# Kernel tuning notes

Measured on AMD Instinct MI355X. Metric: run time of the kernel, lower is better.

## Reference

```python
import jax, jax.numpy as jnp
import numpy as np

JACCARD_THRESH = 0.5
NEGPOS_RATIO = 3
V0, V1 = 0.1, 0.2  # SSD encoding variances


def setup_inputs() -> dict:
    key = jax.random.key(0)
    k1, k2, k3, k4, k5, k6, k7 = jax.random.split(key, 7)
    B, P, C, O = 128, 8732, 21, 16
    loc_data = jax.random.normal(k1, (B, P, 4), dtype=jnp.float32)
    conf_data = jax.random.normal(k2, (B, P, C), dtype=jnp.float32)
    # default boxes in center form (cx, cy, w, h), all in [0,1]
    cxcy = jax.random.uniform(k3, (P, 2), minval=0.05, maxval=0.95)
    wh = jax.random.uniform(k4, (P, 2), minval=0.05, maxval=0.6)
    dbox_list = jnp.concatenate([cxcy, wh], axis=1).astype(jnp.float32)
    # ground-truth boxes in corner form with guaranteed positive extent
    tl = jax.random.uniform(k5, (B, O, 2), minval=0.0, maxval=0.6)
    sz = jax.random.uniform(k6, (B, O, 2), minval=0.05, maxval=0.35)
    labels = jax.random.randint(k7, (B, O, 1), 0, C - 1).astype(jnp.float32)
    targets = jnp.concatenate([tl, tl + sz, labels], axis=2)
    return {"loc_data": loc_data, "conf_data": conf_data,
            "dbox_list": dbox_list, "targets": targets}


def _match_one(truths, labels, dbox):
    """SSD match for one image. truths:[O,4] corner, labels:[O], dbox:[P,4] center."""
    pf = jnp.concatenate([dbox[:, :2] - dbox[:, 2:] * 0.5,
                          dbox[:, :2] + dbox[:, 2:] * 0.5], axis=1)  # point form [P,4]
    lt = jnp.maximum(truths[:, None, :2], pf[None, :, :2])
    rb = jnp.minimum(truths[:, None, 2:], pf[None, :, 2:])
    whi = jnp.clip(rb - lt, 0.0)
    inter = whi[..., 0] * whi[..., 1]                                # [O,P]
    area_t = (truths[:, 2] - truths[:, 0]) * (truths[:, 3] - truths[:, 1])
    area_p = dbox[:, 2] * dbox[:, 3]
    ov = inter / (area_t[:, None] + area_p[None, :] - inter)         # jaccard [O,P]
    best_prior_idx = jnp.argmax(ov, axis=1)                          # [O]
    bto = jnp.max(ov, axis=0)                                        # [P]
    bti = jnp.argmax(ov, axis=0)                                     # [P]
    bto = bto.at[best_prior_idx].set(2.0)
    O = truths.shape[0]
    bti = jax.lax.fori_loop(0, O, lambda j, b: b.at[best_prior_idx[j]].set(j), bti)
    matched = truths[bti]                                            # [P,4]
    conf = labels[bti].astype(jnp.int32) + 1
    conf = jnp.where(bto < JACCARD_THRESH, 0, conf)
    g_cxcy = ((matched[:, :2] + matched[:, 2:]) * 0.5 - dbox[:, :2]) / (V0 * dbox[:, 2:])
    g_wh = jnp.log((matched[:, 2:] - matched[:, :2]) / dbox[:, 2:]) / V1
    return jnp.concatenate([g_cxcy, g_wh], axis=1), conf


def reference(loc_data, conf_data, dbox_list, targets):
    B, P, C = conf_data.shape
    loc_t, conf_t = jax.vmap(_match_one, in_axes=(0, 0, None))(
        targets[..., :4], targets[..., 4], dbox_list)
    pos = conf_t > 0                                                  # [B,P]
    # smooth L1 (beta=1), summed over positives
    ad = jnp.abs(loc_data - loc_t)
    sl1 = jnp.where(ad < 1.0, 0.5 * ad * ad, ad - 0.5)
    loss_l = jnp.sum(jnp.where(pos[..., None], sl1, 0.0))
    # per-prior cross entropy
    logp = jax.nn.log_softmax(conf_data, axis=-1)
    ce = -jnp.take_along_axis(logp, conf_t[..., None], axis=-1)[..., 0]  # [B,P]
    # hard negative mining via double argsort (rank in descending order)
    ce_neg = jnp.where(pos, 0.0, ce)
    loss_idx = jnp.argsort(-ce_neg, axis=1)
    idx_rank = jnp.argsort(loss_idx, axis=1)
    num_pos = jnp.sum(pos, axis=1, keepdims=True)
    num_neg = jnp.minimum(num_pos * NEGPOS_RATIO, P)
    neg = idx_rank < num_neg
    sel = pos | neg
    loss_c = jnp.sum(jnp.where(sel, ce, 0.0))
    N = jnp.sum(num_pos).astype(loc_data.dtype)
    return jnp.stack([loss_l / N, loss_c / N])
```

## Files before the change

kernel.cpp:

```cpp
#include <hip/hip_runtime.h>
#include <cstddef>

#define Bn 128
#define Pn 8732
#define Cn 21
#define On 16
#define MAGIC 0x13579BDFu

__device__ __forceinline__ void argmax_combine(float& v, int& p, float v2, int p2) {
  if (v2 > v || (v2 == v && p2 < p)) { v = v2; p = p2; }
}

__global__ __launch_bounds__(256) void stream_kernel(
    const float* __restrict__ conf, const float* __restrict__ dbox,
    const float* __restrict__ targets,
    float* __restrict__ ce0, unsigned char* __restrict__ pack,
    unsigned long long* __restrict__ keys) {
  const int wb = threadIdx.x >> 6, lane = threadIdx.x & 63;
  const int wave_g = blockIdx.x * 4 + wb;
  const int b = wave_g & 127;
  const int cg = wave_g >> 7;

  __shared__ float4 s_row4[4][336];
  __shared__ float s_tt[4][On * 5];
  __shared__ float s_ar[4][On];

  #pragma unroll
  for (int i = lane; i < On * 5; i += 64)
    s_tt[wb][i] = targets[(size_t)b * On * 5 + i];
  if (lane < On) {
    float x1 = targets[(size_t)b * On * 5 + lane * 5 + 0];
    float y1 = targets[(size_t)b * On * 5 + lane * 5 + 1];
    float x2 = targets[(size_t)b * On * 5 + lane * 5 + 2];
    float y2 = targets[(size_t)b * On * 5 + lane * 5 + 3];
    s_ar[wb][lane] = (x2 - x1) * (y2 - y1);
  }

  float bestv[On]; int bestp[On];
  #pragma unroll
  for (int j = 0; j < On; j++) { bestv[j] = -1.0f; bestp[j] = 0x7fffffff; }

  #pragma unroll
  for (int i = 0; i < 3; i++) {
    const int ci = cg + 64 * i;
    if (ci >= 137) break;
    const int p0 = ci * 64;
    const int rows = min(64, Pn - p0);
    const int n4 = rows * Cn / 4;

    const float4* src = (const float4*)(conf + ((size_t)b * Pn + p0) * Cn);
    float4 v0, v1, v2, v3, v4, v5;
    if (lane < n4)        v0 = src[lane];
    if (lane + 64 < n4)   v1 = src[lane + 64];
    if (lane + 128 < n4)  v2 = src[lane + 128];
    if (lane + 192 < n4)  v3 = src[lane + 192];
    if (lane + 256 < n4)  v4 = src[lane + 256];
    if (lane + 320 < n4)  v5 = src[lane + 320];
    if (lane < n4)        s_row4[wb][lane] = v0;
    if (lane + 64 < n4)   s_row4[wb][lane + 64] = v1;
    if (lane + 128 < n4)  s_row4[wb][lane + 128] = v2;
    if (lane + 192 < n4)  s_row4[wb][lane + 192] = v3;
    if (lane + 256 < n4)  s_row4[wb][lane + 256] = v4;
    if (lane + 320 < n4)  s_row4[wb][lane + 320] = v5;

    if (lane < rows) {
      const int p = p0 + lane;
      const float* x = (const float*)s_row4[wb] + lane * Cn;
      float m = x[0];
      #pragma unroll
      for (int q = 1; q < Cn; q++) m = fmaxf(m, x[q]);
      float s = 0.0f;
      #pragma unroll
      for (int q = 0; q < Cn; q++) s += __expf(x[q] - m);
      float lse = m + __logf(s);
      ce0[(size_t)b * Pn + p] = lse - x[0];

      float4 d = ((const float4*)dbox)[p];
      float px1 = d.x - d.z * 0.5f, py1 = d.y - d.w * 0.5f;
      float px2 = d.x + d.z * 0.5f, py2 = d.y + d.w * 0.5f;
      float ap = d.z * d.w;
      float mv = -1.0f; int mj = 0;
      #pragma unroll
      for (int j = 0; j < On; j++) {
        float lx = fmaxf(s_tt[wb][j*5+0], px1);
        float ly = fmaxf(s_tt[wb][j*5+1], py1);
        float rx = fminf(s_tt[wb][j*5+2], px2);
        float ry = fminf(s_tt[wb][j*5+3], py2);
        float w = fmaxf(rx - lx, 0.0f), h = fmaxf(ry - ly, 0.0f);
        float inter = w * h;
        float ov = __fdividef(inter, s_ar[wb][j] + ap - inter);
        if (ov > bestv[j]) { bestv[j] = ov; bestp[j] = p; }
        if (ov > mv) { mv = ov; mj = j; }
      }
      pack[(size_t)b * Pn + p] =
          (unsigned char)(mj | ((mv >= 0.5f) ? 16 : 0));
    }
  }

  #pragma unroll
  for (int j = 0; j < On; j++) {
    float v = bestv[j]; int p = bestp[j];
    #pragma unroll
    for (int off = 32; off; off >>= 1) {
      float v2 = __shfl_down(v, off);
      int p2 = __shfl_down(p, off);
      argmax_combine(v, p, v2, p2);
    }
    if (lane == 0) {
      unsigned long long key;
      if (v < 0.0f) key = 0xC000000000000000ull;
      else key = (((unsigned long long)(__float_as_uint(v) | 0xC0000000u)) << 32)
               | (unsigned long long)(0xFFFFFFFFu - (unsigned)p);
      atomicMax(&keys[b * On + j], key);
    }
  }
}

__global__ __launch_bounds__(1024) void reduce_kernel(
    const float* __restrict__ loc, const float* __restrict__ conf,
    const float* __restrict__ dbox, const float* __restrict__ targets,
    const float* __restrict__ ce0, const unsigned char* __restrict__ pack,
    const unsigned long long* __restrict__ keys,
    unsigned int* __restrict__ res, float* __restrict__ out) {
  const int b = blockIdx.x;
  const int tid = threadIdx.x;
  const int wave = tid >> 6, lane = tid & 63;

  __shared__ float s_t[On * 5];
  __shared__ int s_bp[On];
  __shared__ unsigned hist[256 * 16];
  __shared__ unsigned s_col[256];
  __shared__ unsigned s_cand[64];
  __shared__ float s_redf[2][16];
  __shared__ int s_redi[16];
  __shared__ unsigned s_prefix;
  __shared__ int s_kk;
  __shared__ int s_cnt;
  __shared__ int s_cc;
  __shared__ int s_np;

  if (tid < On * 5) s_t[tid] = targets[(size_t)b * On * 5 + tid];
  if (tid < On)
    s_bp[tid] = (int)(0xFFFFFFFFu - (unsigned)(keys[b * On + tid] & 0xFFFFFFFFull));
  __syncthreads();

  float ce_r[9];
  float my_loc = 0.0f, my_cep = 0.0f; int my_np = 0;
  #pragma unroll
  for (int sI = 0; sI < 9; sI++) {
    ce_r[sI] = 0.0f;
    const int p = tid + 1024 * sI;
    if (p < Pn) {
      unsigned char pk = pack[(size_t)b * Pn + p];
      float c0 = ce0[(size_t)b * Pn + p];
      int pos = pk >> 4;
      int bt = pk & 15;
      #pragma unroll
      for (int j = 0; j < On; j++)
        if (s_bp[j] == p) { bt = j; pos = 1; }
      ce_r[sI] = pos ? 0.0f : c0;
      if (pos) {
        my_np++;
        const float* t = &s_t[bt * 5];
        int c = (int)t[4] + 1;
        const float* row = conf + ((size_t)b * Pn + p) * Cn;
        my_cep += c0 + row[0] - row[c];
        float4 d = ((const float4*)dbox)[p];
        float mx1 = t[0], my1 = t[1], mx2 = t[2], my2 = t[3];
        float g0 = ((mx1 + mx2) * 0.5f - d.x) / (0.1f * d.z);
        float g1 = ((my1 + my2) * 0.5f - d.y) / (0.1f * d.w);
        float g2 = logf((mx2 - mx1) / d.z) / 0.2f;
        float g3 = logf((my2 - my1) / d.w) / 0.2f;
        float4 ld = ((const float4*)loc)[(size_t)b * Pn + p];
        float g[4] = {g0, g1, g2, g3};
        float l[4] = {ld.x, ld.y, ld.z, ld.w};
        #pragma unroll
        for (int q = 0; q < 4; q++) {
          float ad = fabsf(l[q] - g[q]);
          my_loc += (ad < 1.0f) ? 0.5f * ad * ad : ad - 0.5f;
        }
      }
    }
  }

  {
    int np = my_np;
    #pragma unroll
    for (int off = 32; off; off >>= 1) np += __shfl_down(np, off);
    if (lane == 0) s_redi[wave] = np;
  }
  __syncthreads();
  if (tid == 0) {
    int np = 0;
    #pragma unroll
    for (int w = 0; w < 16; w++) np += s_redi[w];
    s_np = np;
  }
  __syncthreads();

  const int k = min(s_np * 3, Pn);
  unsigned prefix = 0, maskb = 0;
  int kk = k;
  int cntc = Pn;
  for (int shift = 24; shift >= 0; shift -= 8) {
    if (cntc <= 64) break;
    ((uint4*)hist)[tid] = make_uint4(0u, 0u, 0u, 0u);
    __syncthreads();
    #pragma unroll
    for (int sI = 0; sI < 9; sI++) {
      const int p = tid + 1024 * sI;
      if (p < Pn) {
        unsigned u = __float_as_uint(ce_r[sI]);
        if ((u & maskb) == prefix)
          atomicAdd(&hist[(((u >> shift) & 255u) << 4) + (unsigned)wave], 1u);
      }
    }
    __syncthreads();
    if (tid < 256) {
      unsigned c = 0;
      #pragma unroll
      for (int w = 0; w < 16; w++) c += hist[(tid << 4) + w];
      s_col[tid] = c;
    }
    __syncthreads();
    if (tid < 64) {
      unsigned c0 = s_col[4 * tid + 0], c1 = s_col[4 * tid + 1];
      unsigned c2 = s_col[4 * tid + 2], c3 = s_col[4 * tid + 3];
      unsigned t0 = c0 + c1 + c2 + c3;
      unsigned S = t0;
      #pragma unroll
      for (int off = 1; off < 64; off <<= 1) {
        unsigned o = __shfl_down(S, off);
        if (tid + off < 64) S += o;
      }
      unsigned Snext = S - t0;
      unsigned s3 = Snext + c3;
      unsigned s2 = s3 + c2;
      unsigned s1 = s2 + c1;
      unsigned s0 = s1 + c0;
      unsigned kk_u = (unsigned)kk;
      int chosen = -1; unsigned snx = 0, cc = 0;
      if (s3 >= kk_u && Snext < kk_u)      { chosen = 3; snx = Snext; cc = c3; }
      else if (s2 >= kk_u && s3 < kk_u)    { chosen = 2; snx = s3;    cc = c2; }
      else if (s1 >= kk_u && s2 < kk_u)    { chosen = 1; snx = s2;    cc = c1; }
      else if (s0 >= kk_u && s1 < kk_u)    { chosen = 0; snx = s1;    cc = c0; }
      if (chosen >= 0) {
        s_prefix = prefix | ((unsigned)(4 * tid + chosen) << shift);
        s_kk = (int)(kk_u - snx);
        s_cnt = (int)cc;
      }
    }
    __syncthreads();
    prefix = s_prefix; kk = s_kk; cntc = s_cnt;
    maskb |= 255u << shift;
  }
  if (maskb != 0xFFFFFFFFu) {
    if (tid == 0) s_cc = 0;
    __syncthreads();
    #pragma unroll
    for (int sI = 0; sI < 9; sI++) {
      const int p = tid + 1024 * sI;
      if (p < Pn) {
        unsigned u = __float_as_uint(ce_r[sI]);
        if ((u & maskb) == prefix) {
          int ix = atomicAdd(&s_cc, 1);
          s_cand[ix] = u;
        }
      }
    }
    __syncthreads();
    if (tid < 64) {
      int c = s_cc;
      if (tid < c) {
        unsigned v = s_cand[tid];
        int g = 0, e = 0;
        for (int i = 0; i < c; i++) {
          unsigned w = s_cand[i];
          g += (w > v); e += (w == v);
        }
        if (g < kk && kk <= g + e) s_prefix = v;
      }
    }
    __syncthreads();
    prefix = s_prefix;
  }
  float T = __uint_as_float(prefix);

  float sum_gt = 0.0f; int cnt_gt = 0;
  #pragma unroll
  for (int sI = 0; sI < 9; sI++) {
    const int p = tid + 1024 * sI;
    if (p < Pn) {
      float x = ce_r[sI];
      if (x > T) { sum_gt += x; cnt_gt++; }
    }
  }
  #pragma unroll
  for (int off = 32; off; off >>= 1) {
    sum_gt += __shfl_down(sum_gt, off);
    cnt_gt += __shfl_down(cnt_gt, off);
    my_loc += __shfl_down(my_loc, off);
    my_cep += __shfl_down(my_cep, off);
  }
  if (lane == 0) {
    s_redf[0][wave] = my_loc; s_redf[1][wave] = sum_gt + my_cep; s_redi[wave] = cnt_gt;
  }
  __syncthreads();
  if (tid == 0) {
    float ll = 0.0f, lc = 0.0f; int cg = 0;
    #pragma unroll
    for (int w = 0; w < 16; w++) {
      ll += s_redf[0][w]; lc += s_redf[1][w]; cg += s_redi[w];
    }
    lc += (k > 0) ? (float)(k - cg) * T : 0.0f;
    atomicExch(&res[b * 4 + 0], __float_as_uint(ll));
    atomicExch(&res[b * 4 + 1], __float_as_uint(lc));
    atomicExch(&res[b * 4 + 2], (unsigned)s_np);
    __threadfence();
    atomicExch(&res[b * 4 + 3], MAGIC);
  }

  if (b == 0 && tid < 64) {
    float ll = 0.0f, lc = 0.0f; int np = 0;
    #pragma unroll
    for (int h = 0; h < 2; h++) {
      const int i = tid + 64 * h;
      while (atomicAdd(&res[i * 4 + 3], 0u) != MAGIC) { __builtin_amdgcn_s_sleep(8); }
      ll += __uint_as_float(atomicAdd(&res[i * 4 + 0], 0u));
      lc += __uint_as_float(atomicAdd(&res[i * 4 + 1], 0u));
      np += (int)atomicAdd(&res[i * 4 + 2], 0u);
    }
    #pragma unroll
    for (int off = 32; off; off >>= 1) {
      ll += __shfl_down(ll, off);
      lc += __shfl_down(lc, off);
      np += __shfl_down(np, off);
    }
    if (tid == 0) {
      float fN = (float)np;
      out[0] = ll / fN;
      out[1] = lc / fN;
    }
  }
}

extern "C" void kernel_launch(void* const* d_in, const int* in_sizes, int n_in,
                              void* d_out, int out_size, void* d_ws, size_t ws_size,
                              hipStream_t stream) {
  const float* loc_data  = (const float*)d_in[0];
  const float* conf_data = (const float*)d_in[1];
  const float* dbox      = (const float*)d_in[2];
  const float* targets   = (const float*)d_in[3];
  float* out = (float*)d_out;

  char* ws = (char*)d_ws;
  float* ce0 = (float*)ws;
  unsigned char* pack = (unsigned char*)(ws + (size_t)Bn * Pn * 4);
  unsigned long long* keys =
      (unsigned long long*)(ws + (size_t)Bn * Pn * 5);
  unsigned int* res = (unsigned int*)(ws + (size_t)Bn * Pn * 5 + Bn * On * 8);

  stream_kernel<<<2048, 256, 0, stream>>>(conf_data, dbox, targets, ce0, pack, keys);
  reduce_kernel<<<Bn, 1024, 0, stream>>>(loc_data, conf_data, dbox, targets,
                                         ce0, pack, keys, res, out);
}
```

Baseline: 205.2 us.

## Software-pipeline conf chunk loads in registers ahead of compute in stream kernel

Restructures the per-wave chunk loop so the global loads for the first two conf chunks are issued up front into register buffers, and the third chunk's load is issued before the second chunk is computed. This lets global memory latency overlap with the softmax and IoU compute instead of being serialized per chunk. Target loads are also hoisted into registers before the conf loads and written to shared memory afterward. The cost is higher register pressure from holding two 6-float4 buffers, which may reduce occupancy.

Measured after the change: 252.4 us. +23.0%, slower.

```diff
diff --git a/kernel.cpp b/kernel.cpp
--- a/kernel.cpp
+++ b/kernel.cpp
@@ -25,44 +25,58 @@
   __shared__ float s_tt[4][On * 5];
   __shared__ float s_ar[4][On];
 
-  #pragma unroll
-  for (int i = lane; i < On * 5; i += 64)
-    s_tt[wb][i] = targets[(size_t)b * On * 5 + i];
+  const size_t tb = (size_t)b * On * 5;
+  float tva = targets[tb + lane];
+  float tvb = 0.0f, ax1 = 0.0f, ay1 = 0.0f, ax2 = 0.0f, ay2 = 0.0f;
   if (lane < On) {
-    float x1 = targets[(size_t)b * On * 5 + lane * 5 + 0];
-    float y1 = targets[(size_t)b * On * 5 + lane * 5 + 1];
-    float x2 = targets[(size_t)b * On * 5 + lane * 5 + 2];
-    float y2 = targets[(size_t)b * On * 5 + lane * 5 + 3];
-    s_ar[wb][lane] = (x2 - x1) * (y2 - y1);
-  }
-
-  float bestv[On]; int bestp[On];
-  #pragma unroll
-  for (int j = 0; j < On; j++) { bestv[j] = -1.0f; bestp[j] = 0x7fffffff; }
-
-  #pragma unroll
-  for (int i = 0; i < 3; i++) {
-    const int ci = cg + 64 * i;
-    if (ci >= 137) break;
+    tvb = targets[tb + 64 + lane];
+    ax1 = targets[tb + lane * 5 + 0];
+    ay1 = targets[tb + lane * 5 + 1];
+    ax2 = targets[tb + lane * 5 + 2];
+    ay2 = targets[tb + lane * 5 + 3];
+  }
+
+  float4 ra[6], rb[6];
+  auto LOADR = [&](float4 (&r)[6], int ci) {
     const int p0 = ci * 64;
     const int rows = min(64, Pn - p0);
     const int n4 = rows * Cn / 4;
-
     const float4* src = (const float4*)(conf + ((size_t)b * Pn + p0) * Cn);
-    float4 v0, v1, v2, v3, v4, v5;
-    if (lane < n4)        v0 = src[lane];
-    if (lane + 64 < n4)   v1 = src[lane + 64];
-    if (lane + 128 < n4)  v2 = src[lane + 128];
-    if (lane + 192 < n4)  v3 = src[lane + 192];
-    if (lane + 256 < n4)  v4 = src[lane + 256];
-    if (lane + 320 < n4)  v5 = src[lane + 320];
-    if (lane < n4)        s_row4[wb][lane] = v0;
-    if (lane + 64 < n4)   s_row4[wb][lane + 64] = v1;
-    if (lane + 128 < n4)  s_row4[wb][lane + 128] = v2;
-    if (lane + 192 < n4)  s_row4[wb][lane + 192] = v3;
-    if (lane + 256 < n4)  s_row4[wb][lane + 256] = v4;
-    if (lane + 320 < n4)  s_row4[wb][lane + 320] = v5;
-
+    if (lane < n4)        r[0] = src[lane];
+    if (lane + 64 < n4)   r[1] = src[lane + 64];
+    if (lane + 128 < n4)  r[2] = src[lane + 128];
+    if (lane + 192 < n4)  r[3] = src[lane + 192];
+    if (lane + 256 < n4)  r[4] = src[lane + 256];
+    if (lane + 320 < n4)  r[5] = src[lane + 320];
+  };
+  auto WRITER = [&](const float4 (&r)[6], int ci) {
+    const int p0 = ci * 64;
+    const int rows = min(64, Pn - p0);
+    const int n4 = rows * Cn / 4;
+    if (lane < n4)        s_row4[wb][lane] = r[0];
+    if (lane + 64 < n4)   s_row4[wb][lane + 64] = r[1];
+    if (lane + 128 < n4)  s_row4[wb][lane + 128] = r[2];
+    if (lane + 192 < n4)  s_row4[wb][lane + 192] = r[3];
+    if (lane + 256 < n4)  s_row4[wb][lane + 256] = r[4];
+    if (lane + 320 < n4)  s_row4[wb][lane + 320] = r[5];
+  };
+
+  LOADR(ra, cg);
+  LOADR(rb, cg + 64);
+
+  s_tt[wb][lane] = tva;
+  if (lane < On) {
+    s_tt[wb][64 + lane] = tvb;
+    s_ar[wb][lane] = (ax2 - ax1) * (ay2 - ay1);
+  }
+
+  float bestv[On]; int bestp[On];
+  #pragma unroll
+  for (int j = 0; j < On; j++) { bestv[j] = -1.0f; bestp[j] = 0x7fffffff; }
+
+  auto COMPUTE = [&](int ci) {
+    const int p0 = ci * 64;
+    const int rows = min(64, Pn - p0);
     if (lane < rows) {
       const int p = p0 + lane;
       const float* x = (const float*)s_row4[wb] + lane * Cn;
@@ -95,7 +109,15 @@
       pack[(size_t)b * Pn + p] =
           (unsigned char)(mj | ((mv >= 0.5f) ? 16 : 0));
     }
-  }
+  };
+
+  WRITER(ra, cg);
+  COMPUTE(cg);
+  WRITER(rb, cg + 64);
+  const bool has2 = (cg < 9);
+  if (has2) LOADR(ra, cg + 128);
+  COMPUTE(cg + 64);
+  if (has2) { WRITER(ra, cg + 128); COMPUTE(cg + 128); }
 
   #pragma unroll
   for (int j = 0; j < On; j++) {
```

## Fuse stream and reduce kernels via last-arriving-block per-image reduction

Applied to the files above, without the earlier changes.

Merges the two kernels into one launch. The last wave to finish streaming an image, found with an atomic counter, runs that image's top-k reduction inside a 256-thread block. A second counter picks the final block to do the global sum. The stream grid shrinks from 64 to 32 waves per image, each covering up to 5 chunks, and shared memory is overlaid with a union. The aim is to remove the kernel-launch gap and the spin-wait, but the per-image reduction now runs with 256 threads instead of 1024 and adds a memset. Key buffers are not reset, as before.

New measurement: 436.2 us. +112.6%, slower.

```diff
diff --git a/kernel.cpp b/kernel.cpp
--- a/kernel.cpp
+++ b/kernel.cpp
@@ -5,151 +5,55 @@
 #define Pn 8732
 #define Cn 21
 #define On 16
-#define MAGIC 0x13579BDFu
+#define NW 32
+#define NI 35
 
 __device__ __forceinline__ void argmax_combine(float& v, int& p, float v2, int p2) {
   if (v2 > v || (v2 == v && p2 < p)) { v = v2; p = p2; }
 }
 
-__global__ __launch_bounds__(256) void stream_kernel(
-    const float* __restrict__ conf, const float* __restrict__ dbox,
-    const float* __restrict__ targets,
-    float* __restrict__ ce0, unsigned char* __restrict__ pack,
-    unsigned long long* __restrict__ keys) {
-  const int wb = threadIdx.x >> 6, lane = threadIdx.x & 63;
-  const int wave_g = blockIdx.x * 4 + wb;
-  const int b = wave_g & 127;
-  const int cg = wave_g >> 7;
-
-  __shared__ float4 s_row4[4][336];
-  __shared__ float s_tt[4][On * 5];
-  __shared__ float s_ar[4][On];
-
-  #pragma unroll
-  for (int i = lane; i < On * 5; i += 64)
-    s_tt[wb][i] = targets[(size_t)b * On * 5 + i];
-  if (lane < On) {
-    float x1 = targets[(size_t)b * On * 5 + lane * 5 + 0];
-    float y1 = targets[(size_t)b * On * 5 + lane * 5 + 1];
-    float x2 = targets[(size_t)b * On * 5 + lane * 5 + 2];
-    float y2 = targets[(size_t)b * On * 5 + lane * 5 + 3];
-    s_ar[wb][lane] = (x2 - x1) * (y2 - y1);
-  }
-
-  float bestv[On]; int bestp[On];
-  #pragma unroll
-  for (int j = 0; j < On; j++) { bestv[j] = -1.0f; bestp[j] = 0x7fffffff; }
-
-  #pragma unroll
-  for (int i = 0; i < 3; i++) {
-    const int ci = cg + 64 * i;
-    if (ci >= 137) break;
-    const int p0 = ci * 64;
-    const int rows = min(64, Pn - p0);
-    const int n4 = rows * Cn / 4;
-
-    const float4* src = (const float4*)(conf + ((size_t)b * Pn + p0) * Cn);
-    float4 v0, v1, v2, v3, v4, v5;
-    if (lane < n4)        v0 = src[lane];
-    if (lane + 64 < n4)   v1 = src[lane + 64];
-    if (lane + 128 < n4)  v2 = src[lane + 128];
-    if (lane + 192 < n4)  v3 = src[lane + 192];
-    if (lane + 256 < n4)  v4 = src[lane + 256];
-    if (lane + 320 < n4)  v5 = src[lane + 320];
-    if (lane < n4)        s_row4[wb][lane] = v0;
-    if (lane + 64 < n4)   s_row4[wb][lane + 64] = v1;
-    if (lane + 128 < n4)  s_row4[wb][lane + 128] = v2;
-    if (lane + 192 < n4)  s_row4[wb][lane + 192] = v3;
-    if (lane + 256 < n4)  s_row4[wb][lane + 256] = v4;
-    if (lane + 320 < n4)  s_row4[wb][lane + 320] = v5;
-
-    if (lane < rows) {
-      const int p = p0 + lane;
-      const float* x = (const float*)s_row4[wb] + lane * Cn;
-      float m = x[0];
-      #pragma unroll
-      for (int q = 1; q < Cn; q++) m = fmaxf(m, x[q]);
-      float s = 0.0f;
-      #pragma unroll
-      for (int q = 0; q < Cn; q++) s += __expf(x[q] - m);
-      float lse = m + __logf(s);
-      ce0[(size_t)b * Pn + p] = lse - x[0];
-
-      float4 d = ((const float4*)dbox)[p];
-      float px1 = d.x - d.z * 0.5f, py1 = d.y - d.w * 0.5f;
-      float px2 = d.x + d.z * 0.5f, py2 = d.y + d.w * 0.5f;
-      float ap = d.z * d.w;
-      float mv = -1.0f; int mj = 0;
-      #pragma unroll
-      for (int j = 0; j < On; j++) {
-        float lx = fmaxf(s_tt[wb][j*5+0], px1);
-        float ly = fmaxf(s_tt[wb][j*5+1], py1);
-        float rx = fminf(s_tt[wb][j*5+2], px2);
-        float ry = fminf(s_tt[wb][j*5+3], py2);
-        float w = fmaxf(rx - lx, 0.0f), h = fmaxf(ry - ly, 0.0f);
-        float inter = w * h;
-        float ov = __fdividef(inter, s_ar[wb][j] + ap - inter);
-        if (ov > bestv[j]) { bestv[j] = ov; bestp[j] = p; }
-        if (ov > mv) { mv = ov; mj = j; }
-      }
-      pack[(size_t)b * Pn + p] =
-          (unsigned char)(mj | ((mv >= 0.5f) ? 16 : 0));
-    }
-  }
-
-  #pragma unroll
-  for (int j = 0; j < On; j++) {
-    float v = bestv[j]; int p = bestp[j];
-    #pragma unroll
-    for (int off = 32; off; off >>= 1) {
-      float v2 = __shfl_down(v, off);
-      int p2 = __shfl_down(p, off);
-      argmax_combine(v, p, v2, p2);
-    }
-    if (lane == 0) {
-      unsigned long long key;
-      if (v < 0.0f) key = 0xC000000000000000ull;
-      else key = (((unsigned long long)(__float_as_uint(v) | 0xC0000000u)) << 32)
-               | (unsigned long long)(0xFFFFFFFFu - (unsigned)p);
-      atomicMax(&keys[b * On + j], key);
-    }
-  }
-}
-
-__global__ __launch_bounds__(1024) void reduce_kernel(
+union SmemU {
+  struct {
+    float4 row4[4][336];
+    float  tt[4][On * 5];
+    float  ar[4][On];
+  } st;
+  struct {
+    unsigned hist[256 * 4];
+    unsigned col[256];
+    unsigned cand[64];
+    float    t[On * 5];
+    int      bp[On];
+    float    redf[2][4];
+    int      redi[4];
+    unsigned prefix;
+    int      kk, cnt, cc, np, fin;
+  } rd;
+};
+
+__device__ void reduce_image(
+    int b, SmemU& u,
     const float* __restrict__ loc, const float* __restrict__ conf,
     const float* __restrict__ dbox, const float* __restrict__ targets,
     const float* __restrict__ ce0, const unsigned char* __restrict__ pack,
     const unsigned long long* __restrict__ keys,
-    unsigned int* __restrict__ res, float* __restrict__ out) {
-  const int b = blockIdx.x;
+    unsigned* res, unsigned* done2, float* out) {
   const int tid = threadIdx.x;
   const int wave = tid >> 6, lane = tid & 63;
 
-  __shared__ float s_t[On * 5];
-  __shared__ int s_bp[On];
-  __shared__ unsigned hist[256 * 16];
-  __shared__ unsigned s_col[256];
-  __shared__ unsigned s_cand[64];
-  __shared__ float s_redf[2][16];
-  __shared__ int s_redi[16];
-  __shared__ unsigned s_prefix;
-  __shared__ int s_kk;
-  __shared__ int s_cnt;
-  __shared__ int s_cc;
-  __shared__ int s_np;
-
-  if (tid < On * 5) s_t[tid] = targets[(size_t)b * On * 5 + tid];
+  __threadfence();
+
+  if (tid < On * 5) u.rd.t[tid] = targets[(size_t)b * On * 5 + tid];
   if (tid < On)
-    s_bp[tid] = (int)(0xFFFFFFFFu - (unsigned)(keys[b * On + tid] & 0xFFFFFFFFull));
-  __syncthreads();
-
-  float ce_r[9];
+    u.rd.bp[tid] = (int)(0xFFFFFFFFu - (unsigned)(keys[b * On + tid] & 0xFFFFFFFFull));
+  __syncthreads();
+
+  float ce_r[NI];
   float my_loc = 0.0f, my_cep = 0.0f; int my_np = 0;
   #pragma unroll
-  for (int sI = 0; sI < 9; sI++) {
+  for (int sI = 0; sI < NI; sI++) {
     ce_r[sI] = 0.0f;
-    const int p = tid + 1024 * sI;
+    const int p = tid + 256 * sI;
     if (p < Pn) {
       unsigned char pk = pack[(size_t)b * Pn + p];
       float c0 = ce0[(size_t)b * Pn + p];
@@ -157,11 +61,11 @@
       int bt = pk & 15;
       #pragma unroll
       for (int j = 0; j < On; j++)
-        if (s_bp[j] == p) { bt = j; pos = 1; }
+        if (u.rd.bp[j] == p) { bt = j; pos = 1; }
       ce_r[sI] = pos ? 0.0f : c0;
       if (pos) {
         my_np++;
-        const float* t = &s_t[bt * 5];
+        const float* t = &u.rd.t[bt * 5];
         int c = (int)t[4] + 1;
         const float* row = conf + ((size_t)b * Pn + p) * Cn;
         my_cep += c0 + row[0] - row[c];
@@ -187,45 +91,40 @@
     int np = my_np;
     #pragma unroll
     for (int off = 32; off; off >>= 1) np += __shfl_down(np, off);
-    if (lane == 0) s_redi[wave] = np;
-  }
-  __syncthreads();
-  if (tid == 0) {
-    int np = 0;
-    #pragma unroll
-    for (int w = 0; w < 16; w++) np += s_redi[w];
-    s_np = np;
-  }
-  __syncthreads();
-
-  const int k = min(s_np * 3, Pn);
+    if (lane == 0) u.rd.redi[wave] = np;
+  }
+  __syncthreads();
+  if (tid == 0)
+    u.rd.np = u.rd.redi[0] + u.rd.redi[1] + u.rd.redi[2] + u.rd.redi[3];
+  __syncthreads();
+
+  const int k = min(u.rd.np * 3, Pn);
   unsigned prefix = 0, maskb = 0;
   int kk = k;
   int cntc = Pn;
   for (int shift = 24; shift >= 0; shift -= 8) {
     if (cntc <= 64) break;
-    ((uint4*)hist)[tid] = make_uint4(0u, 0u, 0u, 0u);
-    __syncthreads();
-    #pragma unroll
-    for (int sI = 0; sI < 9; sI++) {
-      const int p = tid + 1024 * sI;
+    ((uint4*)u.rd.hist)[tid] = make_uint4(0u, 0u, 0u, 0u);
+    __syncthreads();
+    #pragma unroll
+    for (int sI = 0; sI < NI; sI++) {
+      const int p = tid + 256 * sI;
       if (p < Pn) {
-        unsigned u = __float_as_uint(ce_r[sI]);
-        if ((u & maskb) == prefix)
-          atomicAdd(&hist[(((u >> shift) & 255u) << 4) + (unsigned)wave], 1u);
-      }
-    }
-    __syncthreads();
-    if (tid < 256) {
-      unsigned c = 0;
-      #pragma unroll
-      for (int w = 0; w < 16; w++) c += hist[(tid << 4) + w];
-      s_col[tid] = c;
+        unsigned uu = __float_as_uint(ce_r[sI]);
+        if ((uu & maskb) == prefix)
+          atomicAdd(&u.rd.hist[(((uu >> shift) & 255u) << 2) + (unsigned)wave], 1u);
+      }
+    }
+    __syncthreads();
+    {
+      unsigned c = u.rd.hist[tid * 4 + 0] + u.rd.hist[tid * 4 + 1] +
+                   u.rd.hist[tid * 4 + 2] + u.rd.hist[tid * 4 + 3];
+      u.rd.col[tid] = c;
     }
     __syncthreads();
     if (tid < 64) {
-      unsigned c0 = s_col[4 * tid + 0], c1 = s_col[4 * tid + 1];
-      unsigned c2 = s_col[4 * tid + 2], c3 = s_col[4 * tid + 3];
+      unsigned c0 = u.rd.col[4 * tid + 0], c1 = u.rd.col[4 * tid + 1];
+      unsigned c2 = u.rd.col[4 * tid + 2], c3 = u.rd.col[4 * tid + 3];
       unsigned t0 = c0 + c1 + c2 + c3;
       unsigned S = t0;
       #pragma unroll
@@ -245,51 +144,51 @@
       else if (s1 >= kk_u && s2 < kk_u)    { chosen = 1; snx = s2;    cc = c1; }
       else if (s0 >= kk_u && s1 < kk_u)    { chosen = 0; snx = s1;    cc = c0; }
       if (chosen >= 0) {
-        s_prefix = prefix | ((unsigned)(4 * tid + chosen) << shift);
-        s_kk = (int)(kk_u - snx);
-        s_cnt = (int)cc;
-      }
-    }
-    __syncthreads();
-    prefix = s_prefix; kk = s_kk; cntc = s_cnt;
+        u.rd.prefix = prefix | ((unsigned)(4 * tid + chosen) << shift);
+        u.rd.kk = (int)(kk_u - snx);
+        u.rd.cnt = (int)cc;
+      }
+    }
+    __syncthreads();
+    prefix = u.rd.prefix; kk = u.rd.kk; cntc = u.rd.cnt;
     maskb |= 255u << shift;
   }
   if (maskb != 0xFFFFFFFFu) {
-    if (tid == 0) s_cc = 0;
-    __syncthreads();
-    #pragma unroll
-    for (int sI = 0; sI < 9; sI++) {
-      const int p = tid + 1024 * sI;
+    if (tid == 0) u.rd.cc = 0;
+    __syncthreads();
+    #pragma unroll
+    for (int sI = 0; sI < NI; sI++) {
+      const int p = tid + 256 * sI;
       if (p < Pn) {
-        unsigned u = __float_as_uint(ce_r[sI]);
-        if ((u & maskb) == prefix) {
-          int ix = atomicAdd(&s_cc, 1);
-          s_cand[ix] = u;
+        unsigned uu = __float_as_uint(ce_r[sI]);
+        if ((uu & maskb) == prefix) {
+          int ix = atomicAdd(&u.rd.cc, 1);
+          u.rd.cand[ix] = uu;
         }
       }
     }
     __syncthreads();
     if (tid < 64) {
-      int c = s_cc;
+      int c = u.rd.cc;
       if (tid < c) {
-        unsigned v = s_cand[tid];
+        unsigned v = u.rd.cand[tid];
         int g = 0, e = 0;
         for (int i = 0; i < c; i++) {
-          unsigned w = s_cand[i];
+          unsigned w = u.rd.cand[i];
           g += (w > v); e += (w == v);
         }
-        if (g < kk && kk <= g + e) s_prefix = v;
-      }
-    }
-    __syncthreads();
-    prefix = s_prefix;
+        if (g < kk && kk <= g + e) u.rd.prefix = v;
+      }
+    }
+    __syncthreads();
+    prefix = u.rd.prefix;
   }
   float T = __uint_as_float(prefix);
 
   float sum_gt = 0.0f; int cnt_gt = 0;
   #pragma unroll
-  for (int sI = 0; sI < 9; sI++) {
-    const int p = tid + 1024 * sI;
+  for (int sI = 0; sI < NI; sI++) {
+    const int p = tid + 256 * sI;
     if (p < Pn) {
       float x = ce_r[sI];
       if (x > T) { sum_gt += x; cnt_gt++; }
@@ -303,32 +202,33 @@
     my_cep += __shfl_down(my_cep, off);
   }
   if (lane == 0) {
-    s_redf[0][wave] = my_loc; s_redf[1][wave] = sum_gt + my_cep; s_redi[wave] = cnt_gt;
+    u.rd.redf[0][wave] = my_loc;
+    u.rd.redf[1][wave] = sum_gt + my_cep;
+    u.rd.redi[wave] = cnt_gt;
   }
   __syncthreads();
   if (tid == 0) {
-    float ll = 0.0f, lc = 0.0f; int cg = 0;
-    #pragma unroll
-    for (int w = 0; w < 16; w++) {
-      ll += s_redf[0][w]; lc += s_redf[1][w]; cg += s_redi[w];
-    }
-    lc += (k > 0) ? (float)(k - cg) * T : 0.0f;
+    float ll = 0.0f, lc = 0.0f; int cg2 = 0;
+    #pragma unroll
+    for (int w = 0; w < 4; w++) {
+      ll += u.rd.redf[0][w]; lc += u.rd.redf[1][w]; cg2 += u.rd.redi[w];
+    }
+    lc += (k > 0) ? (float)(k - cg2) * T : 0.0f;
     atomicExch(&res[b * 4 + 0], __float_as_uint(ll));
     atomicExch(&res[b * 4 + 1], __float_as_uint(lc));
-    atomicExch(&res[b * 4 + 2], (unsigned)s_np);
+    atomicExch(&res[b * 4 + 2], (unsigned)u.rd.np);
     __threadfence();
-    atomicExch(&res[b * 4 + 3], MAGIC);
-  }
-
-  if (b == 0 && tid < 64) {
+    unsigned o2 = atomicAdd(done2, 1u);
+    u.rd.fin = (o2 == (unsigned)(Bn - 1)) ? 1 : 0;
+  }
+  __syncthreads();
+  if (u.rd.fin) {
+    __threadfence();
     float ll = 0.0f, lc = 0.0f; int np = 0;
-    #pragma unroll
-    for (int h = 0; h < 2; h++) {
-      const int i = tid + 64 * h;
-      while (atomicAdd(&res[i * 4 + 3], 0u) != MAGIC) { __builtin_amdgcn_s_sleep(8); }
-      ll += __uint_as_float(atomicAdd(&res[i * 4 + 0], 0u));
-      lc += __uint_as_float(atomicAdd(&res[i * 4 + 1], 0u));
-      np += (int)atomicAdd(&res[i * 4 + 2], 0u);
+    if (tid < Bn) {
+      ll = __uint_as_float(atomicAdd(&res[tid * 4 + 0], 0u));
+      lc = __uint_as_float(atomicAdd(&res[tid * 4 + 1], 0u));
+      np = (int)atomicAdd(&res[tid * 4 + 2], 0u);
     }
     #pragma unroll
     for (int off = 32; off; off >>= 1) {
@@ -336,11 +236,140 @@
       lc += __shfl_down(lc, off);
       np += __shfl_down(np, off);
     }
+    if (lane == 0 && wave < 2) {
+      u.rd.redf[0][wave] = ll; u.rd.redf[1][wave] = lc; u.rd.redi[wave] = np;
+    }
+    __syncthreads();
     if (tid == 0) {
-      float fN = (float)np;
-      out[0] = ll / fN;
-      out[1] = lc / fN;
-    }
+      float L = u.rd.redf[0][0] + u.rd.redf[0][1];
+      float C = u.rd.redf[1][0] + u.rd.redf[1][1];
+      float N = (float)(u.rd.redi[0] + u.rd.redi[1]);
+      out[0] = L / N;
+      out[1] = C / N;
+    }
+  }
+  __syncthreads();
+}
+
+__global__ __launch_bounds__(256) void fused_kernel(
+    const float* __restrict__ loc, const float* __restrict__ conf,
+    const float* __restrict__ dbox, const float* __restrict__ targets,
+    float* __restrict__ ce0, unsigned char* __restrict__ pack,
+    unsigned long long* __restrict__ keys,
+    unsigned* __restrict__ res, float* __restrict__ out) {
+  const int wb = threadIdx.x >> 6, lane = threadIdx.x & 63;
+  const int wave_g = blockIdx.x * 4 + wb;
+  const int b = wave_g & 127;
+  const int cg = wave_g >> 7;
+
+  unsigned* done  = res + Bn * 4;
+  unsigned* done2 = done + Bn;
+
+  __shared__ SmemU u;
+  __shared__ int s_job[4];
+
+  #pragma unroll
+  for (int i = lane; i < On * 5; i += 64)
+    u.st.tt[wb][i] = targets[(size_t)b * On * 5 + i];
+  if (lane < On) {
+    float x1 = targets[(size_t)b * On * 5 + lane * 5 + 0];
+    float y1 = targets[(size_t)b * On * 5 + lane * 5 + 1];
+    float x2 = targets[(size_t)b * On * 5 + lane * 5 + 2];
+    float y2 = targets[(size_t)b * On * 5 + lane * 5 + 3];
+    u.st.ar[wb][lane] = (x2 - x1) * (y2 - y1);
+  }
+
+  float bestv[On]; int bestp[On];
+  #pragma unroll
+  for (int j = 0; j < On; j++) { bestv[j] = -1.0f; bestp[j] = 0x7fffffff; }
+
+  #pragma unroll
+  for (int i = 0; i < 5; i++) {
+    const int ci = cg + 32 * i;
+    if (ci >= 137) break;
+    const int p0 = ci * 64;
+    const int rows = min(64, Pn - p0);
+    const int n4 = rows * Cn / 4;
+
+    const float4* src = (const float4*)(conf + ((size_t)b * Pn + p0) * Cn);
+    float4 v0, v1, v2, v3, v4, v5;
+    if (lane < n4)        v0 = src[lane];
+    if (lane + 64 < n4)   v1 = src[lane + 64];
+    if (lane + 128 < n4)  v2 = src[lane + 128];
+    if (lane + 192 < n4)  v3 = src[lane + 192];
+    if (lane + 256 < n4)  v4 = src[lane + 256];
+    if (lane + 320 < n4)  v5 = src[lane + 320];
+    if (lane < n4)        u.st.row4[wb][lane] = v0;
+    if (lane + 64 < n4)   u.st.row4[wb][lane + 64] = v1;
+    if (lane + 128 < n4)  u.st.row4[wb][lane + 128] = v2;
+    if (lane + 192 < n4)  u.st.row4[wb][lane + 192] = v3;
+    if (lane + 256 < n4)  u.st.row4[wb][lane + 256] = v4;
+    if (lane + 320 < n4)  u.st.row4[wb][lane + 320] = v5;
+
+    if (lane < rows) {
+      const int p = p0 + lane;
+      const float* x = (const float*)u.st.row4[wb] + lane * Cn;
+      float m = x[0];
+      #pragma unroll
+      for (int q = 1; q < Cn; q++) m = fmaxf(m, x[q]);
+      float s = 0.0f;
+      #pragma unroll
+      for (int q = 0; q < Cn; q++) s += __expf(x[q] - m);
+      float lse = m + __logf(s);
+      ce0[(size_t)b * Pn + p] = lse - x[0];
+
+      float4 d = ((const float4*)dbox)[p];
+      float px1 = d.x - d.z * 0.5f, py1 = d.y - d.w * 0.5f;
+      float px2 = d.x + d.z * 0.5f, py2 = d.y + d.w * 0.5f;
+      float ap = d.z * d.w;
+      float mv = -1.0f; int mj = 0;
+      #pragma unroll
+      for (int j = 0; j < On; j++) {
+        float lx = fmaxf(u.st.tt[wb][j*5+0], px1);
+        float ly = fmaxf(u.st.tt[wb][j*5+1], py1);
+        float rx = fminf(u.st.tt[wb][j*5+2], px2);
+        float ry = fminf(u.st.tt[wb][j*5+3], py2);
+        float w = fmaxf(rx - lx, 0.0f), h = fmaxf(ry - ly, 0.0f);
+        float inter = w * h;
+        float ov = __fdividef(inter, u.st.ar[wb][j] + ap - inter);
+        if (ov > bestv[j]) { bestv[j] = ov; bestp[j] = p; }
+        if (ov > mv) { mv = ov; mj = j; }
+      }
+      pack[(size_t)b * Pn + p] =
+          (unsigned char)(mj | ((mv >= 0.5f) ? 16 : 0));
+    }
+  }
+
+  #pragma unroll
+  for (int j = 0; j < On; j++) {
+    float v = bestv[j]; int p = bestp[j];
+    #pragma unroll
+    for (int off = 32; off; off >>= 1) {
+      float v2 = __shfl_down(v, off);
+      int p2 = __shfl_down(p, off);
+      argmax_combine(v, p, v2, p2);
+    }
+    if (lane == 0) {
+      unsigned long long key;
+      if (v < 0.0f) key = 0xC000000000000000ull;
+      else key = (((unsigned long long)(__float_as_uint(v) | 0xC0000000u)) << 32)
+               | (unsigned long long)(0xFFFFFFFFu - (unsigned)p);
+      atomicMax(&keys[b * On + j], key);
+    }
+  }
+
+  if (lane == 0) {
+    __threadfence();
+    unsigned old = atomicAdd(&done[b], 1u);
+    s_job[wb] = (old == (unsigned)(NW - 1)) ? b : -1;
+  }
+  __syncthreads();
+
+  for (int s = 0; s < 4; ++s) {
+    const int img = s_job[s];
+    if (img >= 0)
+      reduce_image(img, u, loc, conf, dbox, targets, ce0, pack, keys,
+                   res, done2, out);
   }
 }
 
@@ -358,9 +387,11 @@
   unsigned char* pack = (unsigned char*)(ws + (size_t)Bn * Pn * 4);
   unsigned long long* keys =
       (unsigned long long*)(ws + (size_t)Bn * Pn * 5);
-  unsigned int* res = (unsigned int*)(ws + (size_t)Bn * Pn * 5 + Bn * On * 8);
-
-  stream_kernel<<<2048, 256, 0, stream>>>(conf_data, dbox, targets, ce0, pack, keys);
-  reduce_kernel<<<Bn, 1024, 0, stream>>>(loc_data, conf_data, dbox, targets,
-                                         ce0, pack, keys, res, out);
+  unsigned int* res =
+      (unsigned int*)(ws + (size_t)Bn * Pn * 5 + Bn * On * 8);
+
+  hipMemsetAsync(res, 0, (size_t)(Bn * 4 + Bn + 1) * sizeof(unsigned), stream);
+
+  fused_kernel<<<Bn * NW / 4, 256, 0, stream>>>(
+      loc_data, conf_data, dbox, targets, ce0, pack, keys, res, out);
 }
```

## Fuse positive-prior loss accumulation into stream kernel and vectorize reduce pass

Applied to the files above, without the earlier changes.

Positive-prior localization and confidence losses are now computed in the streaming kernel while the conf row is already in shared memory, and accumulated per image with atomics. The reduce kernel only corrects for the forced best-prior matches and loads ce0 as float4 instead of re-scanning pack, conf and loc per prior. Grid size is halved so each wave processes more chunks. This adds a memset, float atomics (non-deterministic summation order) and a correction path for duplicate best-prior indices.

Result: slower. 210.3 us (+2.5%).

```diff
diff --git a/kernel.cpp b/kernel.cpp
--- a/kernel.cpp
+++ b/kernel.cpp
@@ -11,11 +11,25 @@
   if (v2 > v || (v2 == v && p2 < p)) { v = v2; p = p2; }
 }
 
+__device__ __forceinline__ float sl1_enc(float4 lv, float4 d,
+                                         float t0, float t1, float t2, float t3) {
+  float g0 = ((t0 + t2) * 0.5f - d.x) / (0.1f * d.z);
+  float g1 = ((t1 + t3) * 0.5f - d.y) / (0.1f * d.w);
+  float g2 = __logf((t2 - t0) / d.z) / 0.2f;
+  float g3 = __logf((t3 - t1) / d.w) / 0.2f;
+  float r = 0.f, a;
+  a = fabsf(lv.x - g0); r += (a < 1.f) ? 0.5f * a * a : a - 0.5f;
+  a = fabsf(lv.y - g1); r += (a < 1.f) ? 0.5f * a * a : a - 0.5f;
+  a = fabsf(lv.z - g2); r += (a < 1.f) ? 0.5f * a * a : a - 0.5f;
+  a = fabsf(lv.w - g3); r += (a < 1.f) ? 0.5f * a * a : a - 0.5f;
+  return r;
+}
+
 __global__ __launch_bounds__(256) void stream_kernel(
-    const float* __restrict__ conf, const float* __restrict__ dbox,
-    const float* __restrict__ targets,
+    const float* __restrict__ loc, const float* __restrict__ conf,
+    const float* __restrict__ dbox, const float* __restrict__ targets,
     float* __restrict__ ce0, unsigned char* __restrict__ pack,
-    unsigned long long* __restrict__ keys) {
+    unsigned long long* __restrict__ keys, unsigned* __restrict__ part) {
   const int wb = threadIdx.x >> 6, lane = threadIdx.x & 63;
   const int wave_g = blockIdx.x * 4 + wb;
   const int b = wave_g & 127;
@@ -25,7 +39,6 @@
   __shared__ float s_tt[4][On * 5];
   __shared__ float s_ar[4][On];
 
-  #pragma unroll
   for (int i = lane; i < On * 5; i += 64)
     s_tt[wb][i] = targets[(size_t)b * On * 5 + i];
   if (lane < On) {
@@ -40,9 +53,11 @@
   #pragma unroll
   for (int j = 0; j < On; j++) { bestv[j] = -1.0f; bestp[j] = 0x7fffffff; }
 
-  #pragma unroll
-  for (int i = 0; i < 3; i++) {
-    const int ci = cg + 64 * i;
+  float acc_loc = 0.0f, acc_cep = 0.0f; int acc_np = 0;
+
+  #pragma unroll
+  for (int i = 0; i < 5; i++) {
+    const int ci = cg + 32 * i;
     if (ci >= 137) break;
     const int p0 = ci * 64;
     const int rows = min(64, Pn - p0);
@@ -73,7 +88,6 @@
       #pragma unroll
       for (int q = 0; q < Cn; q++) s += __expf(x[q] - m);
       float lse = m + __logf(s);
-      ce0[(size_t)b * Pn + p] = lse - x[0];
 
       float4 d = ((const float4*)dbox)[p];
       float px1 = d.x - d.z * 0.5f, py1 = d.y - d.w * 0.5f;
@@ -92,9 +106,31 @@
         if (ov > bestv[j]) { bestv[j] = ov; bestp[j] = p; }
         if (ov > mv) { mv = ov; mj = j; }
       }
-      pack[(size_t)b * Pn + p] =
-          (unsigned char)(mj | ((mv >= 0.5f) ? 16 : 0));
-    }
+      const bool pos = (mv >= 0.5f);
+      pack[(size_t)b * Pn + p] = (unsigned char)(mj | (pos ? 16 : 0));
+      ce0[(size_t)b * Pn + p] = pos ? 0.0f : (lse - x[0]);
+
+      if (pos) {
+        acc_np++;
+        int c = (int)s_tt[wb][mj * 5 + 4] + 1;
+        acc_cep += lse - x[c];
+        float4 lv = ((const float4*)loc)[(size_t)b * Pn + p];
+        acc_loc += sl1_enc(lv, d, s_tt[wb][mj*5+0], s_tt[wb][mj*5+1],
+                                  s_tt[wb][mj*5+2], s_tt[wb][mj*5+3]);
+      }
+    }
+  }
+
+  #pragma unroll
+  for (int off = 32; off; off >>= 1) {
+    acc_loc += __shfl_down(acc_loc, off);
+    acc_cep += __shfl_down(acc_cep, off);
+    acc_np  += __shfl_down(acc_np, off);
+  }
+  if (lane == 0) {
+    atomicAdd((float*)&part[b * 4 + 0], acc_loc);
+    atomicAdd((float*)&part[b * 4 + 1], acc_cep);
+    atomicAdd(&part[b * 4 + 2], (unsigned)acc_np);
   }
 
   #pragma unroll
@@ -121,6 +157,7 @@
     const float* __restrict__ dbox, const float* __restrict__ targets,
     const float* __restrict__ ce0, const unsigned char* __restrict__ pack,
     const unsigned long long* __restrict__ keys,
+    const unsigned* __restrict__ part,
     unsigned int* __restrict__ res, float* __restrict__ out) {
   const int b = blockIdx.x;
   const int tid = threadIdx.x;
@@ -128,92 +165,116 @@
 
   __shared__ float s_t[On * 5];
   __shared__ int s_bp[On];
+  __shared__ unsigned s_pk[On];
+  __shared__ int s_fp[On];
   __shared__ unsigned hist[256 * 16];
   __shared__ unsigned s_col[256];
   __shared__ unsigned s_cand[64];
-  __shared__ float s_redf[2][16];
+  __shared__ float s_redf[16];
   __shared__ int s_redi[16];
   __shared__ unsigned s_prefix;
   __shared__ int s_kk;
   __shared__ int s_cnt;
+  __shared__ int s_cc2;
   __shared__ int s_cc;
   __shared__ int s_np;
+  __shared__ float s_ltot, s_ctot;
 
   if (tid < On * 5) s_t[tid] = targets[(size_t)b * On * 5 + tid];
-  if (tid < On)
-    s_bp[tid] = (int)(0xFFFFFFFFu - (unsigned)(keys[b * On + tid] & 0xFFFFFFFFull));
+  if (tid < On) {
+    int bp = (int)(0xFFFFFFFFu - (unsigned)(keys[b * On + tid] & 0xFFFFFFFFull));
+    s_bp[tid] = bp;
+    s_pk[tid] = pack[(size_t)b * Pn + bp];
+  }
+  if (tid == 1023) s_cc = 0;
   __syncthreads();
 
-  float ce_r[9];
-  float my_loc = 0.0f, my_cep = 0.0f; int my_np = 0;
-  #pragma unroll
-  for (int sI = 0; sI < 9; sI++) {
-    ce_r[sI] = 0.0f;
-    const int p = tid + 1024 * sI;
-    if (p < Pn) {
-      unsigned char pk = pack[(size_t)b * Pn + p];
-      float c0 = ce0[(size_t)b * Pn + p];
-      int pos = pk >> 4;
-      int bt = pk & 15;
-      #pragma unroll
-      for (int j = 0; j < On; j++)
-        if (s_bp[j] == p) { bt = j; pos = 1; }
-      ce_r[sI] = pos ? 0.0f : c0;
-      if (pos) {
-        my_np++;
-        const float* t = &s_t[bt * 5];
-        int c = (int)t[4] + 1;
-        const float* row = conf + ((size_t)b * Pn + p) * Cn;
-        my_cep += c0 + row[0] - row[c];
-        float4 d = ((const float4*)dbox)[p];
-        float mx1 = t[0], my1 = t[1], mx2 = t[2], my2 = t[3];
-        float g0 = ((mx1 + mx2) * 0.5f - d.x) / (0.1f * d.z);
-        float g1 = ((my1 + my2) * 0.5f - d.y) / (0.1f * d.w);
-        float g2 = logf((mx2 - mx1) / d.z) / 0.2f;
-        float g3 = logf((my2 - my1) / d.w) / 0.2f;
-        float4 ld = ((const float4*)loc)[(size_t)b * Pn + p];
-        float g[4] = {g0, g1, g2, g3};
-        float l[4] = {ld.x, ld.y, ld.z, ld.w};
-        #pragma unroll
-        for (int q = 0; q < 4; q++) {
-          float ad = fabsf(l[q] - g[q]);
-          my_loc += (ad < 1.0f) ? 0.5f * ad * ad : ad - 0.5f;
-        }
-      }
-    }
-  }
-
-  {
-    int np = my_np;
-    #pragma unroll
-    for (int off = 32; off; off >>= 1) np += __shfl_down(np, off);
-    if (lane == 0) s_redi[wave] = np;
+  if (wave == 0) {
+    const bool valid = lane < On;
+    const int p = valid ? s_bp[lane] : 0;
+    bool dup = false;
+    if (valid)
+      for (int j2 = lane + 1; j2 < On; j2++) dup |= (s_bp[j2] == p);
+    const bool act = valid && !dup;
+    float dloc = 0.f, dcep = 0.f; int dnp = 0;
+    if (act) {
+      const unsigned pk = s_pk[lane];
+      const int pos0 = pk >> 4, mjo = pk & 15;
+      const float* row = conf + ((size_t)b * Pn + p) * Cn;
+      float xr[Cn];
+      #pragma unroll
+      for (int q = 0; q < Cn; q++) xr[q] = row[q];
+      float m = xr[0];
+      #pragma unroll
+      for (int q = 1; q < Cn; q++) m = fmaxf(m, xr[q]);
+      float s = 0.f;
+      #pragma unroll
+      for (int q = 0; q < Cn; q++) s += __expf(xr[q] - m);
+      const float lse = m + __logf(s);
+      const float4 d = ((const float4*)dbox)[p];
+      const float4 lv = ((const float4*)loc)[(size_t)b * Pn + p];
+      const int cn = (int)s_t[lane * 5 + 4] + 1;
+      dcep = lse - xr[cn];
+      dloc = sl1_enc(lv, d, s_t[lane*5+0], s_t[lane*5+1],
+                            s_t[lane*5+2], s_t[lane*5+3]);
+      if (pos0) {
+        const int co = (int)s_t[mjo * 5 + 4] + 1;
+        dcep -= lse - xr[co];
+        dloc -= sl1_enc(lv, d, s_t[mjo*5+0], s_t[mjo*5+1],
+                              s_t[mjo*5+2], s_t[mjo*5+3]);
+      } else {
+        dnp = 1;
+        int ix = atomicAdd(&s_cc, 1);
+        if (ix < On) s_fp[ix] = p;
+      }
+    }
+    #pragma unroll
+    for (int off = 32; off; off >>= 1) {
+      dloc += __shfl_down(dloc, off);
+      dcep += __shfl_down(dcep, off);
+      dnp  += __shfl_down(dnp, off);
+    }
+    if (lane == 0) {
+      s_ltot = __uint_as_float(part[b * 4 + 0]) + dloc;
+      s_ctot = __uint_as_float(part[b * 4 + 1]) + dcep;
+      s_np = (int)part[b * 4 + 2] + dnp;
+    }
   }
   __syncthreads();
-  if (tid == 0) {
-    int np = 0;
-    #pragma unroll
-    for (int w = 0; w < 16; w++) np += s_redi[w];
-    s_np = np;
-  }
-  __syncthreads();
+
+  const int ncnt = s_cc;
+  float ce_r[12];
+  #pragma unroll
+  for (int sI = 0; sI < 3; sI++) {
+    const int f = tid + 1024 * sI;
+    float4 v = make_float4(0.f, 0.f, 0.f, 0.f);
+    if (f < Pn / 4) v = ((const float4*)ce0)[(size_t)b * (Pn / 4) + f];
+    ce_r[4*sI+0] = v.x; ce_r[4*sI+1] = v.y; ce_r[4*sI+2] = v.z; ce_r[4*sI+3] = v.w;
+  }
+  for (int i = 0; i < ncnt; i++) {
+    const int fp = s_fp[i];
+    #pragma unroll
+    for (int sI = 0; sI < 3; sI++) {
+      const int f = tid + 1024 * sI;
+      #pragma unroll
+      for (int q = 0; q < 4; q++)
+        if (4 * f + q == fp) ce_r[4*sI+q] = 0.f;
+    }
+  }
 
   const int k = min(s_np * 3, Pn);
   unsigned prefix = 0, maskb = 0;
   int kk = k;
-  int cntc = Pn;
+  int cntc = 12288;
   for (int shift = 24; shift >= 0; shift -= 8) {
     if (cntc <= 64) break;
     ((uint4*)hist)[tid] = make_uint4(0u, 0u, 0u, 0u);
     __syncthreads();
     #pragma unroll
-    for (int sI = 0; sI < 9; sI++) {
-      const int p = tid + 1024 * sI;
-      if (p < Pn) {
-        unsigned u = __float_as_uint(ce_r[sI]);
-        if ((u & maskb) == prefix)
-          atomicAdd(&hist[(((u >> shift) & 255u) << 4) + (unsigned)wave], 1u);
-      }
+    for (int r = 0; r < 12; r++) {
+      unsigned u = __float_as_uint(ce_r[r]);
+      if ((u & maskb) == prefix)
+        atomicAdd(&hist[(((u >> shift) & 255u) << 4) + (unsigned)wave], 1u);
     }
     __syncthreads();
     if (tid < 256) {
@@ -255,22 +316,19 @@
     maskb |= 255u << shift;
   }
   if (maskb != 0xFFFFFFFFu) {
-    if (tid == 0) s_cc = 0;
-    __syncthreads();
-    #pragma unroll
-    for (int sI = 0; sI < 9; sI++) {
-      const int p = tid + 1024 * sI;
-      if (p < Pn) {
-        unsigned u = __float_as_uint(ce_r[sI]);
-        if ((u & maskb) == prefix) {
-          int ix = atomicAdd(&s_cc, 1);
-          s_cand[ix] = u;
-        }
+    if (tid == 0) s_cc2 = 0;
+    __syncthreads();
+    #pragma unroll
+    for (int r = 0; r < 12; r++) {
+      unsigned u = __float_as_uint(ce_r[r]);
+      if ((u & maskb) == prefix) {
+        int ix = atomicAdd(&s_cc2, 1);
+        if (ix < 64) s_cand[ix] = u;
       }
     }
     __syncthreads();
     if (tid < 64) {
-      int c = s_cc;
+      int c = min(s_cc2, 64);
       if (tid < c) {
         unsigned v = s_cand[tid];
         int g = 0, e = 0;
@@ -288,32 +346,23 @@
 
   float sum_gt = 0.0f; int cnt_gt = 0;
   #pragma unroll
-  for (int sI = 0; sI < 9; sI++) {
-    const int p = tid + 1024 * sI;
-    if (p < Pn) {
-      float x = ce_r[sI];
-      if (x > T) { sum_gt += x; cnt_gt++; }
-    }
+  for (int r = 0; r < 12; r++) {
+    float x = ce_r[r];
+    if (x > T) { sum_gt += x; cnt_gt++; }
   }
   #pragma unroll
   for (int off = 32; off; off >>= 1) {
     sum_gt += __shfl_down(sum_gt, off);
     cnt_gt += __shfl_down(cnt_gt, off);
-    my_loc += __shfl_down(my_loc, off);
-    my_cep += __shfl_down(my_cep, off);
-  }
-  if (lane == 0) {
-    s_redf[0][wave] = my_loc; s_redf[1][wave] = sum_gt + my_cep; s_redi[wave] = cnt_gt;
-  }
+  }
+  if (lane == 0) { s_redf[wave] = sum_gt; s_redi[wave] = cnt_gt; }
   __syncthreads();
   if (tid == 0) {
-    float ll = 0.0f, lc = 0.0f; int cg = 0;
-    #pragma unroll
-    for (int w = 0; w < 16; w++) {
-      ll += s_redf[0][w]; lc += s_redf[1][w]; cg += s_redi[w];
-    }
-    lc += (k > 0) ? (float)(k - cg) * T : 0.0f;
-    atomicExch(&res[b * 4 + 0], __float_as_uint(ll));
+    float sg = 0.0f; int cg2 = 0;
+    #pragma unroll
+    for (int w = 0; w < 16; w++) { sg += s_redf[w]; cg2 += s_redi[w]; }
+    float lc = s_ctot + sg + ((k > 0) ? (float)(k - cg2) * T : 0.0f);
+    atomicExch(&res[b * 4 + 0], __float_as_uint(s_ltot));
     atomicExch(&res[b * 4 + 1], __float_as_uint(lc));
     atomicExch(&res[b * 4 + 2], (unsigned)s_np);
     __threadfence();
@@ -358,9 +407,14 @@
   unsigned char* pack = (unsigned char*)(ws + (size_t)Bn * Pn * 4);
   unsigned long long* keys =
       (unsigned long long*)(ws + (size_t)Bn * Pn * 5);
-  unsigned int* res = (unsigned int*)(ws + (size_t)Bn * Pn * 5 + Bn * On * 8);
-
-  stream_kernel<<<2048, 256, 0, stream>>>(conf_data, dbox, targets, ce0, pack, keys);
+  unsigned int* part =
+      (unsigned int*)(ws + (size_t)Bn * Pn * 5 + (size_t)Bn * On * 8);
+  unsigned int* res = part + Bn * 4;
+
+  hipMemsetAsync(part, 0, (size_t)Bn * 4 * sizeof(unsigned), stream);
+
+  stream_kernel<<<1024, 256, 0, stream>>>(loc_data, conf_data, dbox, targets,
+                                          ce0, pack, keys, part);
   reduce_kernel<<<Bn, 1024, 0, stream>>>(loc_data, conf_data, dbox, targets,
-                                         ce0, pack, keys, res, out);
+                                         ce0, pack, keys, part, res, out);
 }
```
